# Performance work log

Measured on AMD Instinct MI355X. Metric: run time of the kernel, lower is better.

The kernel has to match this reference:

```python
import jax, jax.numpy as jnp
import numpy as np

N_NODES = 50000
N_EDGES = 1600000
IN_FEATS = 128
ENC_H = 20
DEC_H = 64


def setup_inputs() -> dict:
    key = jax.random.key(0)
    ks = jax.random.split(key, 14)
    inp = {}
    inp["x"] = jax.random.normal(ks[0], (N_NODES, IN_FEATS), dtype=jnp.float32)
    inp["edge_index"] = jax.random.randint(ks[1], (2, N_EDGES), 0, N_NODES, dtype=jnp.int64)
    inp["node_id"] = 0
    inp["noise_normal"] = jax.random.normal(ks[2], (N_EDGES, ENC_H), dtype=jnp.float32)
    inp["noise_u"] = jax.random.uniform(ks[3], (N_EDGES, 1), dtype=jnp.float32)
    # parameters (glorot-ish init)
    def lin(k, fan_in, fan_out):
        s = 1.0 / np.sqrt(fan_in)
        return jax.random.uniform(k, (fan_in, fan_out), jnp.float32, -s, s)
    inp["W_gc"] = lin(ks[4], IN_FEATS, ENC_H)
    inp["b_gc"] = jnp.zeros((ENC_H,), jnp.float32)
    inp["W_mu"] = lin(ks[5], 3 * ENC_H, ENC_H)
    inp["b_mu"] = jnp.zeros((ENC_H,), jnp.float32)
    inp["W_var"] = lin(ks[6], 3 * ENC_H, ENC_H)
    inp["b_var"] = jnp.zeros((ENC_H,), jnp.float32)
    inp["W_d1"] = lin(ks[7], ENC_H, DEC_H)
    inp["b_d1"] = jnp.zeros((DEC_H,), jnp.float32)
    inp["W_d2"] = lin(ks[8], DEC_H, 1)
    inp["b_d2"] = jnp.zeros((1,), jnp.float32)
    return inp


def _gcn_conv(x, edge_index, W, b):
    """PyG-style GCNConv: add self-loops, symmetric D^-1/2 (A+I) D^-1/2 norm."""
    n = x.shape[0]
    sl = jnp.arange(n, dtype=edge_index.dtype)
    row = jnp.concatenate([edge_index[0], sl])  # source
    col = jnp.concatenate([edge_index[1], sl])  # target
    xw = x @ W  # [N, H]
    deg = jax.ops.segment_sum(jnp.ones_like(col, dtype=xw.dtype), col, num_segments=n)
    dinv = jnp.where(deg > 0, jax.lax.rsqrt(deg), 0.0)
    norm = dinv[row] * dinv[col]  # [E+N]
    out = jax.ops.segment_sum(xw[row] * norm[:, None], col, num_segments=n)
    return out + b


def reference(x, edge_index, node_id, noise_normal, noise_u,
              W_gc, b_gc, W_mu, b_mu, W_var, b_var, W_d1, b_d1, W_d2, b_d2):
    # GCN encoder
    x1 = jax.nn.relu(_gcn_conv(x, edge_index, W_gc, b_gc))  # [N, H]
    # per-edge concat: [src_embed | dst_embed | node_id_embed]
    rows, cols = edge_index[0], edge_index[1]
    node_embed = jnp.broadcast_to(x1[node_id][None, :], (rows.shape[0], x1.shape[1]))
    x2 = jnp.concatenate([x1[rows], x1[cols], node_embed], axis=1)  # [E, 3H]
    # variational heads + reparameterization
    mu = x2 @ W_mu + b_mu
    sigma = jnp.exp(x2 @ W_var + b_var)
    z = mu + sigma * noise_normal  # [E, H]
    # decoder MLP
    h = jax.nn.relu(z @ W_d1 + b_d1)
    sampling_weights = jax.nn.relu(h @ W_d2 + b_d2)  # [E, 1]
    # gumbel-sigmoid sample (training=True, bias=0.0 -> bias'=1e-4, temperature=1.0)
    bias = 0.0001
    eps = (bias - (1.0 - bias)) * noise_u + (1.0 - bias)
    gate = jnp.log(eps) - jnp.log(1.0 - eps) + sampling_weights
    return jax.nn.sigmoid(gate)
```

## Files before the change

### kernel.cpp

```cpp
#include <hip/hip_runtime.h>

#define NFEAT 128
#define H 20
#define DH 64
#define SCAN_T 1024
#define BE 64
#define CAP 128

typedef __attribute__((ext_vector_type(8))) short short8;
typedef __attribute__((ext_vector_type(4))) float f32x4;

__device__ __forceinline__ unsigned short f2bf(float f) {
    union { float f; unsigned u; } v; v.f = f;
    unsigned r = v.u + 0x7fff + ((v.u >> 16) & 1);
    return (unsigned short)(r >> 16);
}
__device__ __forceinline__ unsigned pk2(unsigned short a, unsigned short b) {
    return (unsigned)a | ((unsigned)b << 16);
}

template <int CTRL>
__device__ __forceinline__ float dpp_add(float x) {
    int y = __builtin_amdgcn_update_dpp(0, __float_as_int(x), CTRL, 0xF, 0xF, true);
    return x + __int_as_float(y);
}
__device__ __forceinline__ float sum16(float x) {
    x = dpp_add<0xB1>(x);
    x = dpp_add<0x4E>(x);
    x = dpp_add<0x124>(x);
    x = dpp_add<0x128>(x);
    return x;
}

__global__ __launch_bounds__(256) void k_prep(const float* __restrict__ Wmu, const float* __restrict__ Wvar,
                                              const float* __restrict__ Wd1,
                                              const float* __restrict__ bmu, const float* __restrict__ bvar,
                                              unsigned short* __restrict__ Bh, unsigned short* __restrict__ Bd1,
                                              float* __restrict__ bcat, int* __restrict__ deg, int N) {
    int t = blockIdx.x * blockDim.x + threadIdx.x;
    if (t < N) deg[t] = 0;
    if (t < 512) {
        int f = t >> 6, l = t & 63;
        int tile = f >> 1, s = f & 1;
        int col = (tile & 1) * 16 + (l & 15);
        const float* W = (tile < 2) ? Wmu : Wvar;
#pragma unroll
        for (int j = 0; j < 8; j++) {
            int k = s * 32 + (l >> 4) * 8 + j;
            float v = (k < 3 * H && col < H) ? W[k * H + col] : 0.f;
            Bh[(size_t)f * 512 + l * 8 + j] = f2bf(v);
        }
    } else if (t < 768) {
        int f = (t - 512) >> 6, l = t & 63;
        int n = f * 16 + (l & 15);
#pragma unroll
        for (int j = 0; j < 8; j++) {
            int k = (l >> 4) * 8 + j;
            float v = (k < H) ? Wd1[k * DH + n] : 0.f;
            Bd1[(size_t)f * 512 + l * 8 + j] = f2bf(v);
        }
    } else if (t < 808) {
        int c = t - 768;
        bcat[c] = (c < H) ? bmu[c] : bvar[c - H];
    }
}

__global__ __launch_bounds__(256) void k_bucket_slots(const int* __restrict__ rows, const int* __restrict__ cols,
                                                      int* __restrict__ deg, int* __restrict__ slots, int E) {
    int e = blockIdx.x * blockDim.x + threadIdx.x;
    if (e >= E) return;
    int c = cols[e];
    int pos = atomicAdd(&deg[c], 1);
    if (pos < CAP) slots[(size_t)c * CAP + pos] = rows[e];
}

__global__ __launch_bounds__(256) void k_deg(const int* __restrict__ cols, int* __restrict__ deg, int E) {
    int t = blockIdx.x * blockDim.x + threadIdx.x;
    if (t < E) atomicAdd(&deg[cols[t]], 1);
}

__global__ __launch_bounds__(SCAN_T) void k_scan(const int* __restrict__ deg, int* __restrict__ offsets,
                                                 int* __restrict__ cursor, int N) {
    __shared__ int sums[SCAN_T];
    int t = threadIdx.x;
    int chunk = (N + SCAN_T - 1) / SCAN_T;
    int beg = t * chunk;
    int end = min(beg + chunk, N);
    int s = 0;
    for (int i = beg; i < end; i++) s += deg[i];
    sums[t] = s;
    __syncthreads();
    for (int off = 1; off < SCAN_T; off <<= 1) {
        int v = (t >= off) ? sums[t - off] : 0;
        __syncthreads();
        sums[t] += v;
        __syncthreads();
    }
    int run = (t == 0) ? 0 : sums[t - 1];
    for (int i = beg; i < end; i++) {
        offsets[i] = run;
        cursor[i] = run;
        run += deg[i];
    }
    if (t == SCAN_T - 1) offsets[N] = sums[SCAN_T - 1];
}

__global__ __launch_bounds__(256) void k_bucket_csr(const int* __restrict__ rows, const int* __restrict__ cols,
                                                    int* __restrict__ cursor, int* __restrict__ srcs, int E) {
    int e = blockIdx.x * blockDim.x + threadIdx.x;
    if (e >= E) return;
    int pos = atomicAdd(&cursor[cols[e]], 1);
    srcs[pos] = rows[e];
}

__global__ __launch_bounds__(256) void k_xw_xs(const float* __restrict__ x, const float* __restrict__ Wgc,
                                               const int* __restrict__ deg,
                                               float* __restrict__ xs, int N) {
    __shared__ float Ws[NFEAT * H];
    for (int i = threadIdx.x; i < NFEAT * H; i += blockDim.x) Ws[i] = Wgc[i];
    __syncthreads();
    int n = blockIdx.x * blockDim.x + threadIdx.x;
    if (n >= N) return;
    float acc[H];
#pragma unroll
    for (int j = 0; j < H; j++) acc[j] = 0.f;
    const float4* x4 = (const float4*)(x + (size_t)n * NFEAT);
#pragma unroll 4
    for (int k4 = 0; k4 < NFEAT / 4; k4++) {
        float4 xv = x4[k4];
#pragma unroll
        for (int s = 0; s < 4; s++) {
            float xk = (s == 0) ? xv.x : (s == 1) ? xv.y : (s == 2) ? xv.z : xv.w;
            const float4* wrow = (const float4*)(Ws + (k4 * 4 + s) * H);
#pragma unroll
            for (int q = 0; q < 5; q++) {
                float4 w = wrow[q];
                acc[q * 4 + 0] += xk * w.x;
                acc[q * 4 + 1] += xk * w.y;
                acc[q * 4 + 2] += xk * w.z;
                acc[q * 4 + 3] += xk * w.w;
            }
        }
    }
    float di = rsqrtf((float)(deg[n] + 1));
    float4* o = (float4*)(xs + (size_t)n * H);
#pragma unroll
    for (int q = 0; q < 5; q++)
        o[q] = make_float4(acc[q * 4 + 0] * di, acc[q * 4 + 1] * di, acc[q * 4 + 2] * di, acc[q * 4 + 3] * di);
}

__device__ __forceinline__ void gather_core(const float* __restrict__ xs, const int* __restrict__ idx,
                                            int beg, int end, int n, int q, int degn,
                                            const float* __restrict__ bgc, unsigned short* __restrict__ x1b) {
    float4 s = ((const float4*)(xs + (size_t)n * H))[q];
#pragma unroll 4
    for (int i = beg; i < end; i++) {
        int r = idx[i];
        float4 v = ((const float4*)(xs + (size_t)r * H))[q];
        s.x += v.x; s.y += v.y; s.z += v.z; s.w += v.w;
    }
    float di = rsqrtf((float)(degn + 1));
    float4 b = ((const float4*)bgc)[q];
    unsigned short o0 = f2bf(fmaxf(di * s.x + b.x, 0.f));
    unsigned short o1 = f2bf(fmaxf(di * s.y + b.y, 0.f));
    unsigned short o2 = f2bf(fmaxf(di * s.z + b.z, 0.f));
    unsigned short o3 = f2bf(fmaxf(di * s.w + b.w, 0.f));
    unsigned* dst = (unsigned*)((char*)x1b + (size_t)n * 40 + q * 8);
    dst[0] = pk2(o0, o1);
    dst[1] = pk2(o2, o3);
}

__global__ __launch_bounds__(256) void k_gather_slots(const float* __restrict__ xs, const int* __restrict__ slots,
                                                      const int* __restrict__ deg, const float* __restrict__ bgc,
                                                      unsigned short* __restrict__ x1b, int N) {
    int t = blockIdx.x * blockDim.x + threadIdx.x;
    if (t >= N * 5) return;
    int n = t / 5;
    int q = t - n * 5;
    int d = min(deg[n], CAP);
    gather_core(xs, slots + (size_t)n * CAP, 0, d, n, q, deg[n], bgc, x1b);
}

__global__ __launch_bounds__(256) void k_gather_csr(const float* __restrict__ xs, const int* __restrict__ srcs,
                                                    const int* __restrict__ offsets, const int* __restrict__ deg,
                                                    const float* __restrict__ bgc,
                                                    unsigned short* __restrict__ x1b, int N) {
    int t = blockIdx.x * blockDim.x + threadIdx.x;
    if (t >= N * 5) return;
    int n = t / 5;
    int q = t - n * 5;
    gather_core(xs, srcs, offsets[n], offsets[n + 1], n, q, deg[n], bgc, x1b);
}

__global__ __launch_bounds__(256) void k_mlp(
    const unsigned short* __restrict__ x1b, const int* __restrict__ rows, const int* __restrict__ cols,
    const int* __restrict__ node_id, const float* __restrict__ noise_n, const float* __restrict__ noise_u,
    const unsigned short* __restrict__ Bh, const unsigned short* __restrict__ Bd1g,
    const float* __restrict__ bcat, const float* __restrict__ b_d1,
    const float* __restrict__ W_d2, const float* __restrict__ b_d2,
    float* __restrict__ out, int E) {

    __shared__ __align__(16) unsigned short BhL[8 * 512];
    __shared__ __align__(16) unsigned short Bd1L[4 * 512];
    __shared__ __align__(16) unsigned short x2s[BE * 72];
    __shared__ __align__(16) unsigned short A2[BE * 40];
    __shared__ float bcatL[40];
    __shared__ float bd1L[DH];
    __shared__ float wd2L[DH];
    __shared__ float uL[BE];
    __shared__ float bd2s;

    int tid = threadIdx.x;
    int e0 = blockIdx.x * BE;

    {
        const uint4* s4 = (const uint4*)Bh;
        uint4* d4 = (uint4*)BhL;
        for (int i = tid; i < 512; i += 256) d4[i] = s4[i];
        s4 = (const uint4*)Bd1g;
        d4 = (uint4*)Bd1L;
        d4[tid] = s4[tid];
        uint4 zz = {0u, 0u, 0u, 0u};
        uint4* a4 = (uint4*)A2;
        a4[tid] = zz;
        if (tid < 64) a4[256 + tid] = zz;
        if (tid < 40) bcatL[tid] = bcat[tid];
        if (tid < DH) {
            bd1L[tid] = b_d1[tid];
            wd2L[tid] = W_d2[tid];
            int e = e0 + tid;
            uL[tid] = noise_u[e < E ? e : 0];
        }
        if (tid == 0) bd2s = b_d2[0];
    }

    {
        int le = tid >> 2, p = tid & 3;
        int e = e0 + le; if (e >= E) e = E - 1;
        int r = rows[e], c = cols[e];
        int nid = node_id[0];
#pragma unroll
        for (int ii = 0; ii < 4; ii++) {
            int i = p + ii * 4;
            unsigned* dst = (unsigned*)((char*)x2s + le * 144 + i * 8);
            if (i < 15) {
                int node = (i < 5) ? r : (i < 10) ? c : nid;
                int cc = (i < 5) ? i : (i < 10) ? i - 5 : i - 10;
                const unsigned* sp = (const unsigned*)((const char*)x1b + (size_t)node * 40 + cc * 8);
                dst[0] = sp[0];
                dst[1] = sp[1];
            } else {
                dst[0] = 0u; dst[1] = 0u;
            }
        }
    }
    __syncthreads();

    int l = tid & 63, w = tid >> 6;
    int m = l & 15, quad = l >> 4;

    f32x4 accs[4];
    {
        const char* arow = (const char*)x2s + (w * 16 + m) * 144 + quad * 16;
        short8 a0 = *(const short8*)(arow);
        short8 a1 = *(const short8*)(arow + 64);
#pragma unroll
        for (int t4 = 0; t4 < 4; t4++) {
            f32x4 acc = {0.f, 0.f, 0.f, 0.f};
            short8 b0 = *(const short8*)((const char*)BhL + (t4 * 2 + 0) * 1024 + l * 16);
            short8 b1 = *(const short8*)((const char*)BhL + (t4 * 2 + 1) * 1024 + l * 16);
            acc = __builtin_amdgcn_mfma_f32_16x16x32_bf16(a0, b0, acc, 0, 0, 0);
            acc = __builtin_amdgcn_mfma_f32_16x16x32_bf16(a1, b1, acc, 0, 0, 0);
            accs[t4] = acc;
        }
    }

    {
        float bm0 = bcatL[m];
        float bv0 = bcatL[20 + m];
        float bm1 = (m < 4) ? bcatL[16 + m] : 0.f;
        float bv1 = (m < 4) ? bcatL[36 + m] : 0.f;
        int erow0 = w * 16 + quad * 4;
#pragma unroll
        for (int r4 = 0; r4 < 4; r4++) {
            int e = e0 + erow0 + r4;
            int ec = (e < E) ? e : 0;
            float z0 = accs[0][r4] + bm0 + expf(accs[2][r4] + bv0) * noise_n[(size_t)ec * H + m];
            *(unsigned short*)((char*)A2 + (erow0 + r4) * 80 + m * 2) = f2bf(z0);
            if (m < 4) {
                float z1 = accs[1][r4] + bm1 + expf(accs[3][r4] + bv1) * noise_n[(size_t)ec * H + 16 + m];
                *(unsigned short*)((char*)A2 + (erow0 + r4) * 80 + (16 + m) * 2) = f2bf(z1);
            }
        }
    }
    __syncthreads();

    {
        short8 a2 = *(const short8*)((const char*)A2 + (w * 16 + m) * 80 + quad * 16);
        float p0 = 0.f, p1 = 0.f, p2 = 0.f, p3 = 0.f;
#pragma unroll
        for (int t4 = 0; t4 < 4; t4++) {
            f32x4 acc = {0.f, 0.f, 0.f, 0.f};
            short8 bb = *(const short8*)((const char*)Bd1L + t4 * 1024 + l * 16);
            acc = __builtin_amdgcn_mfma_f32_16x16x32_bf16(a2, bb, acc, 0, 0, 0);
            int col = t4 * 16 + m;
            float bias = bd1L[col], wo = wd2L[col];
            p0 += fmaxf(acc[0] + bias, 0.f) * wo;
            p1 += fmaxf(acc[1] + bias, 0.f) * wo;
            p2 += fmaxf(acc[2] + bias, 0.f) * wo;
            p3 += fmaxf(acc[3] + bias, 0.f) * wo;
        }
        p0 = sum16(p0); p1 = sum16(p1); p2 = sum16(p2); p3 = sum16(p3);
        if (m < 4) {
            float swv = (m == 0) ? p0 : (m == 1) ? p1 : (m == 2) ? p2 : p3;
            int leo = w * 16 + quad * 4 + m;
            int e = e0 + leo;
            if (e < E) {
                float sw = fmaxf(swv + bd2s, 0.f);
                float u = uL[leo];
                float ev = 0.9999f - 0.9998f * u;
                float gate = logf(ev) - logf(1.f - ev) + sw;
                out[e] = 1.f / (1.f + expf(-gate));
            }
        }
    }
}

extern "C" void kernel_launch(void* const* d_in, const int* in_sizes, int n_in,
                              void* d_out, int out_size, void* d_ws, size_t ws_size,
                              hipStream_t stream) {
    const int N = in_sizes[0] / NFEAT;
    const int E = in_sizes[1] / 2;

    const float* x       = (const float*)d_in[0];
    const int*   ei      = (const int*)d_in[1];
    const int*   rows    = ei;
    const int*   cols    = ei + E;
    const int*   node_id = (const int*)d_in[2];
    const float* noise_n = (const float*)d_in[3];
    const float* noise_u = (const float*)d_in[4];
    const float* Wgc  = (const float*)d_in[5];
    const float* bgc  = (const float*)d_in[6];
    const float* Wmu  = (const float*)d_in[7];
    const float* bmu  = (const float*)d_in[8];
    const float* Wvar = (const float*)d_in[9];
    const float* bvar = (const float*)d_in[10];
    const float* Wd1  = (const float*)d_in[11];
    const float* bd1  = (const float*)d_in[12];
    const float* Wd2  = (const float*)d_in[13];
    const float* bd2  = (const float*)d_in[14];
    float* out = (float*)d_out;

    const int B = 256;
    int gN  = (N + B - 1) / B;
    int gN5 = (N * 5 + B - 1) / B;
    int gE  = (E + B - 1) / B;
    int gM  = (E + BE - 1) / BE;

    char* ws = (char*)d_ws;
    bool slot_path = (ws_size >= (size_t)(200000 + (size_t)N * CAP * 4 + 4000000 + 2000000 + 16384));

    if (slot_path) {
        int*   deg   = (int*)ws;
        int*   slots = (int*)(ws + 200000);
        float* xs    = (float*)(ws + 200000 + (size_t)N * CAP * 4);
        char*  p     = ws + 200000 + (size_t)N * CAP * 4 + 4000000;
        unsigned short* x1b = (unsigned short*)p;
        unsigned short* Bh  = (unsigned short*)(p + 2000000);
        unsigned short* Bd1 = (unsigned short*)(p + 2008192);
        float* bcat  = (float*)(p + 2012288);

        k_prep<<<gN, B, 0, stream>>>(Wmu, Wvar, Wd1, bmu, bvar, Bh, Bd1, bcat, deg, N);
        k_bucket_slots<<<gE, B, 0, stream>>>(rows, cols, deg, slots, E);
        k_xw_xs<<<gN, B, 0, stream>>>(x, Wgc, deg, xs, N);
        k_gather_slots<<<gN5, B, 0, stream>>>(xs, slots, deg, bgc, x1b, N);
        k_mlp<<<gM, B, 0, stream>>>(x1b, rows, cols, node_id, noise_n, noise_u,
                                    Bh, Bd1, bcat, bd1, Wd2, bd2, out, E);
    } else {
        int*   deg     = (int*)ws;
        int*   offsets = (int*)(ws + 200000);
        int*   cursor  = (int*)(ws + 400016);
        int*   srcs    = (int*)(ws + 600016);
        float* xs      = (float*)(ws + 7000016);
        unsigned short* x1b = (unsigned short*)(ws + 11000016);
        unsigned short* Bh  = (unsigned short*)(ws + 13000016);
        unsigned short* Bd1 = (unsigned short*)(ws + 13008208);
        float* bcat    = (float*)(ws + 13012304);

        k_prep<<<gN, B, 0, stream>>>(Wmu, Wvar, Wd1, bmu, bvar, Bh, Bd1, bcat, deg, N);
        k_deg<<<gE, B, 0, stream>>>(cols, deg, E);
        k_scan<<<1, SCAN_T, 0, stream>>>(deg, offsets, cursor, N);
        k_bucket_csr<<<gE, B, 0, stream>>>(rows, cols, cursor, srcs, E);
        k_xw_xs<<<gN, B, 0, stream>>>(x, Wgc, deg, xs, N);
        k_gather_csr<<<gN5, B, 0, stream>>>(xs, srcs, offsets, deg, bgc, x1b, N);
        k_mlp<<<gM, B, 0, stream>>>(x1b, rows, cols, node_id, noise_n, noise_u,
                                    Bh, Bd1, bcat, bd1, Wd2, bd2, out, E);
    }
}
```

Measured before the change: 505.3 us.

## Gather neighbors with 16 lanes per node and prefetch noise in MLP kernel

```diff
diff --git a/kernel.cpp b/kernel.cpp
--- a/kernel.cpp
+++ b/kernel.cpp
@@ -149,47 +149,70 @@
         o[q] = make_float4(acc[q * 4 + 0] * di, acc[q * 4 + 1] * di, acc[q * 4 + 2] * di, acc[q * 4 + 3] * di);
 }
 
-__device__ __forceinline__ void gather_core(const float* __restrict__ xs, const int* __restrict__ idx,
-                                            int beg, int end, int n, int q, int degn,
-                                            const float* __restrict__ bgc, unsigned short* __restrict__ x1b) {
-    float4 s = ((const float4*)(xs + (size_t)n * H))[q];
-#pragma unroll 4
-    for (int i = beg; i < end; i++) {
+__device__ __forceinline__ void gather_core16(const float* __restrict__ xs, const int* __restrict__ idx,
+                                              int beg, int end, int n, int sl, int degn,
+                                              const float* __restrict__ bgc, unsigned short* __restrict__ x1b) {
+    float acc[H];
+    if (sl == 0) {
+        const float4* self = (const float4*)(xs + (size_t)n * H);
+#pragma unroll
+        for (int q = 0; q < 5; q++) {
+            float4 v = self[q];
+            acc[q * 4 + 0] = v.x; acc[q * 4 + 1] = v.y; acc[q * 4 + 2] = v.z; acc[q * 4 + 3] = v.w;
+        }
+    } else {
+#pragma unroll
+        for (int j = 0; j < H; j++) acc[j] = 0.f;
+    }
+#pragma unroll 2
+    for (int i = beg + sl; i < end; i += 16) {
         int r = idx[i];
-        float4 v = ((const float4*)(xs + (size_t)r * H))[q];
-        s.x += v.x; s.y += v.y; s.z += v.z; s.w += v.w;
-    }
-    float di = rsqrtf((float)(degn + 1));
-    float4 b = ((const float4*)bgc)[q];
-    unsigned short o0 = f2bf(fmaxf(di * s.x + b.x, 0.f));
-    unsigned short o1 = f2bf(fmaxf(di * s.y + b.y, 0.f));
-    unsigned short o2 = f2bf(fmaxf(di * s.z + b.z, 0.f));
-    unsigned short o3 = f2bf(fmaxf(di * s.w + b.w, 0.f));
-    unsigned* dst = (unsigned*)((char*)x1b + (size_t)n * 40 + q * 8);
-    dst[0] = pk2(o0, o1);
-    dst[1] = pk2(o2, o3);
+        const float4* p = (const float4*)(xs + (size_t)r * H);
+#pragma unroll
+        for (int q = 0; q < 5; q++) {
+            float4 v = p[q];
+            acc[q * 4 + 0] += v.x; acc[q * 4 + 1] += v.y; acc[q * 4 + 2] += v.z; acc[q * 4 + 3] += v.w;
+        }
+    }
+#pragma unroll
+    for (int j = 0; j < H; j++) acc[j] = sum16(acc[j]);
+    if (sl == 0) {
+        float di = rsqrtf((float)(degn + 1));
+        unsigned o[10];
+#pragma unroll
+        for (int j = 0; j < 10; j++) {
+            float v0 = fmaxf(di * acc[2 * j] + bgc[2 * j], 0.f);
+            float v1 = fmaxf(di * acc[2 * j + 1] + bgc[2 * j + 1], 0.f);
+            o[j] = pk2(f2bf(v0), f2bf(v1));
+        }
+        unsigned* dst = (unsigned*)(x1b + (size_t)n * H);
+        *(uint4*)dst = make_uint4(o[0], o[1], o[2], o[3]);
+        *(uint4*)(dst + 4) = make_uint4(o[4], o[5], o[6], o[7]);
+        *(uint2*)(dst + 8) = make_uint2(o[8], o[9]);
+    }
 }
 
 __global__ __launch_bounds__(256) void k_gather_slots(const float* __restrict__ xs, const int* __restrict__ slots,
                                                       const int* __restrict__ deg, const float* __restrict__ bgc,
                                                       unsigned short* __restrict__ x1b, int N) {
-    int t = blockIdx.x * blockDim.x + threadIdx.x;
-    if (t >= N * 5) return;
-    int n = t / 5;
-    int q = t - n * 5;
-    int d = min(deg[n], CAP);
-    gather_core(xs, slots + (size_t)n * CAP, 0, d, n, q, deg[n], bgc, x1b);
+    int wave = (blockIdx.x * 256 + threadIdx.x) >> 6;
+    int lane = threadIdx.x & 63;
+    int n = wave * 4 + (lane >> 4);
+    if (n >= N) return;
+    int dg = deg[n];
+    int d = min(dg, CAP);
+    gather_core16(xs, slots + (size_t)n * CAP, 0, d, n, lane & 15, dg, bgc, x1b);
 }
 
 __global__ __launch_bounds__(256) void k_gather_csr(const float* __restrict__ xs, const int* __restrict__ srcs,
                                                     const int* __restrict__ offsets, const int* __restrict__ deg,
                                                     const float* __restrict__ bgc,
                                                     unsigned short* __restrict__ x1b, int N) {
-    int t = blockIdx.x * blockDim.x + threadIdx.x;
-    if (t >= N * 5) return;
-    int n = t / 5;
-    int q = t - n * 5;
-    gather_core(xs, srcs, offsets[n], offsets[n + 1], n, q, deg[n], bgc, x1b);
+    int wave = (blockIdx.x * 256 + threadIdx.x) >> 6;
+    int lane = threadIdx.x & 63;
+    int n = wave * 4 + (lane >> 4);
+    if (n >= N) return;
+    gather_core16(xs, srcs, offsets[n], offsets[n + 1], n, lane & 15, deg[n], bgc, x1b);
 }
 
 __global__ __launch_bounds__(256) void k_mlp(
@@ -203,7 +226,7 @@
     __shared__ __align__(16) unsigned short BhL[8 * 512];
     __shared__ __align__(16) unsigned short Bd1L[4 * 512];
     __shared__ __align__(16) unsigned short x2s[BE * 72];
-    __shared__ __align__(16) unsigned short A2[BE * 40];
+    __shared__ __align__(16) unsigned short A2[BE * 44];
     __shared__ float bcatL[40];
     __shared__ float bd1L[DH];
     __shared__ float wd2L[DH];
@@ -212,6 +235,18 @@
 
     int tid = threadIdx.x;
     int e0 = blockIdx.x * BE;
+    int l = tid & 63, w = tid >> 6;
+    int m = l & 15, quad = l >> 4;
+    int erow0 = w * 16 + quad * 4;
+
+    float nz0[4], nz1[4];
+#pragma unroll
+    for (int r4 = 0; r4 < 4; r4++) {
+        int e = e0 + erow0 + r4;
+        int ec = (e < E) ? e : 0;
+        nz0[r4] = noise_n[(size_t)ec * H + m];
+        nz1[r4] = (m < 4) ? noise_n[(size_t)ec * H + 16 + m] : 0.f;
+    }
 
     {
         const uint4* s4 = (const uint4*)Bh;
@@ -220,10 +255,6 @@
         s4 = (const uint4*)Bd1g;
         d4 = (uint4*)Bd1L;
         d4[tid] = s4[tid];
-        uint4 zz = {0u, 0u, 0u, 0u};
-        uint4* a4 = (uint4*)A2;
-        a4[tid] = zz;
-        if (tid < 64) a4[256 + tid] = zz;
         if (tid < 40) bcatL[tid] = bcat[tid];
         if (tid < DH) {
             bd1L[tid] = b_d1[tid];
@@ -246,18 +277,15 @@
             if (i < 15) {
                 int node = (i < 5) ? r : (i < 10) ? c : nid;
                 int cc = (i < 5) ? i : (i < 10) ? i - 5 : i - 10;
-                const unsigned* sp = (const unsigned*)((const char*)x1b + (size_t)node * 40 + cc * 8);
-                dst[0] = sp[0];
-                dst[1] = sp[1];
+                uint2 v = *(const uint2*)((const char*)x1b + (size_t)node * 40 + cc * 8);
+                dst[0] = v.x;
+                dst[1] = v.y;
             } else {
                 dst[0] = 0u; dst[1] = 0u;
             }
         }
     }
     __syncthreads();
-
-    int l = tid & 63, w = tid >> 6;
-    int m = l & 15, quad = l >> 4;
 
     f32x4 accs[4];
     {
@@ -280,23 +308,19 @@
         float bv0 = bcatL[20 + m];
         float bm1 = (m < 4) ? bcatL[16 + m] : 0.f;
         float bv1 = (m < 4) ? bcatL[36 + m] : 0.f;
-        int erow0 = w * 16 + quad * 4;
 #pragma unroll
         for (int r4 = 0; r4 < 4; r4++) {
-            int e = e0 + erow0 + r4;
-            int ec = (e < E) ? e : 0;
-            float z0 = accs[0][r4] + bm0 + expf(accs[2][r4] + bv0) * noise_n[(size_t)ec * H + m];
-            *(unsigned short*)((char*)A2 + (erow0 + r4) * 80 + m * 2) = f2bf(z0);
-            if (m < 4) {
-                float z1 = accs[1][r4] + bm1 + expf(accs[3][r4] + bv1) * noise_n[(size_t)ec * H + 16 + m];
-                *(unsigned short*)((char*)A2 + (erow0 + r4) * 80 + (16 + m) * 2) = f2bf(z1);
-            }
+            float z0 = accs[0][r4] + bm0 + expf(accs[2][r4] + bv0) * nz0[r4];
+            *(unsigned short*)((char*)A2 + (erow0 + r4) * 88 + m * 2) = f2bf(z0);
+            unsigned short z1v = 0;
+            if (m < 4) z1v = f2bf(accs[1][r4] + bm1 + expf(accs[3][r4] + bv1) * nz1[r4]);
+            *(unsigned short*)((char*)A2 + (erow0 + r4) * 88 + (16 + m) * 2) = z1v;
         }
     }
     __syncthreads();
 
     {
-        short8 a2 = *(const short8*)((const char*)A2 + (w * 16 + m) * 80 + quad * 16);
+        short8 a2 = *(const short8*)((const char*)A2 + (w * 16 + m) * 88 + quad * 16);
         float p0 = 0.f, p1 = 0.f, p2 = 0.f, p3 = 0.f;
 #pragma unroll
         for (int t4 = 0; t4 < 4; t4++) {
@@ -353,7 +377,7 @@
 
     const int B = 256;
     int gN  = (N + B - 1) / B;
-    int gN5 = (N * 5 + B - 1) / B;
+    int gG  = (N + 15) / 16;
     int gE  = (E + B - 1) / B;
     int gM  = (E + BE - 1) / BE;
 
@@ -373,7 +397,7 @@
         k_prep<<<gN, B, 0, stream>>>(Wmu, Wvar, Wd1, bmu, bvar, Bh, Bd1, bcat, deg, N);
         k_bucket_slots<<<gE, B, 0, stream>>>(rows, cols, deg, slots, E);
         k_xw_xs<<<gN, B, 0, stream>>>(x, Wgc, deg, xs, N);
-        k_gather_slots<<<gN5, B, 0, stream>>>(xs, slots, deg, bgc, x1b, N);
+        k_gather_slots<<<gG, B, 0, stream>>>(xs, slots, deg, bgc, x1b, N);
         k_mlp<<<gM, B, 0, stream>>>(x1b, rows, cols, node_id, noise_n, noise_u,
                                     Bh, Bd1, bcat, bd1, Wd2, bd2, out, E);
     } else {
@@ -392,7 +416,7 @@
         k_scan<<<1, SCAN_T, 0, stream>>>(deg, offsets, cursor, N);
         k_bucket_csr<<<gE, B, 0, stream>>>(rows, cols, cursor, srcs, E);
         k_xw_xs<<<gN, B, 0, stream>>>(x, Wgc, deg, xs, N);
-        k_gather_csr<<<gN5, B, 0, stream>>>(xs, srcs, offsets, deg, bgc, x1b, N);
+        k_gather_csr<<<gG, B, 0, stream>>>(xs, srcs, offsets, deg, bgc, x1b, N);
         k_mlp<<<gM, B, 0, stream>>>(x1b, rows, cols, node_id, noise_n, noise_u,
                                     Bh, Bd1, bcat, bd1, Wd2, bd2, out, E);
     }
```

New measurement: 471.5 us. 1.07x faster.
